# Performance work log

Hardware: AMD Instinct MI355X
Metric: run time of the kernel (lower is better)

Reference implementation:

```python
import jax, jax.numpy as jnp
import numpy as np

K = 3          # kernel_size
N = K * K      # sampling points per pixel
STRIDE = 1
PAD = 1
DIL = 1


def _conv2d(x, w, b):
    # standard NCHW conv for offset / modulation branches
    y = jax.lax.conv_general_dilated(
        x, w, window_strides=(STRIDE, STRIDE),
        padding=((PAD, PAD), (PAD, PAD)),
        rhs_dilation=(DIL, DIL),
        dimension_numbers=('NCHW', 'OIHW', 'NCHW'))
    return y + b[None, :, None, None]


def setup_inputs() -> dict:
    key = jax.random.key(0)
    ks = jax.random.split(key, 6)
    B, C, H, W, O = 8, 64, 96, 96, 64
    x = jax.random.normal(ks[0], (B, C, H, W), jnp.float32)
    # small random offset/modulation weights so sampling points are off-grid
    offset_w = jax.random.normal(ks[1], (2 * N, C, K, K), jnp.float32) * 0.01
    offset_b = jax.random.normal(ks[2], (2 * N,), jnp.float32) * 0.1
    m_w = jax.random.normal(ks[3], (N, C, K, K), jnp.float32) * 0.01
    m_b = jnp.zeros((N,), jnp.float32)
    # Conv3d(in=C, out=O, kernel=(1,1,N)) weight squeezed to [O, C, N]
    conv_w = jax.random.normal(ks[4], (O, C, N), jnp.float32) * (2.0 / (C * N)) ** 0.5
    conv_b = jnp.zeros((O,), jnp.float32)
    return dict(x=x, offset_w=offset_w, offset_b=offset_b,
                m_w=m_w, m_b=m_b, conv_w=conv_w, conv_b=conv_b)


def _deform_forward(x, offset_w, offset_b, m_w, m_b, conv_w, conv_b):
    B, C, H, W = x.shape
    offset = _conv2d(x, offset_w, offset_b)           # [B, 2n, h, w]
    m = jax.nn.sigmoid(_conv2d(x, m_w, m_b))          # [B, n, h, w]
    xp = jnp.pad(x, ((0, 0), (0, 0), (PAD, PAD), (PAD, PAD)))
    Hp, Wp = xp.shape[2], xp.shape[3]
    off = jnp.transpose(offset, (0, 2, 3, 1))         # [B, h, w, 2n]
    mod = jnp.transpose(m, (0, 2, 3, 1))              # [B, h, w, n]

    # p0: conv-center grid on the padded input; pn: kernel-tap offsets
    st = ((K - 1) // 2) * DIL
    p0_x = jnp.arange(st, Hp - (K // 2) * DIL, STRIDE, dtype=jnp.float32)  # [h]
    p0_y = jnp.arange(st, Wp - (K // 2) * DIL, STRIDE, dtype=jnp.float32)  # [w]
    r = jnp.arange(-((K - 1) // 2) * DIL, (K // 2) * DIL + 1, DIL, dtype=jnp.float32)
    pn_x, pn_y = jnp.meshgrid(r, r, indexing='ij')
    pn_x, pn_y = pn_x.reshape(N), pn_y.reshape(N)

    p_x = off[..., :N] + p0_x[None, :, None, None] + pn_x  # [B, h, w, n]
    p_y = off[..., N:] + p0_y[None, None, :, None] + pn_y

    fl_x = jnp.floor(jax.lax.stop_gradient(p_x))
    fl_y = jnp.floor(jax.lax.stop_gradient(p_y))
    q_tl_x = jnp.clip(fl_x, 0, Hp - 1).astype(jnp.int32)
    q_tl_y = jnp.clip(fl_y, 0, Wp - 1).astype(jnp.int32)
    q_br_x = jnp.clip(fl_x + 1, 0, Hp - 1).astype(jnp.int32)
    q_br_y = jnp.clip(fl_y + 1, 0, Wp - 1).astype(jnp.int32)

    pcx = jnp.clip(p_x, 0, Hp - 1)
    pcy = jnp.clip(p_y, 0, Wp - 1)

    tlx = q_tl_x.astype(pcx.dtype); tly = q_tl_y.astype(pcy.dtype)
    brx = q_br_x.astype(pcx.dtype); bry = q_br_y.astype(pcy.dtype)
    g_tl = (1 + (tlx - pcx)) * (1 + (tly - pcy))
    g_tr = (1 + (tlx - pcx)) * (1 - (bry - pcy))
    g_bl = (1 - (brx - pcx)) * (1 + (tly - pcy))
    g_br = (1 - (brx - pcx)) * (1 - (bry - pcy))

    xflat = xp.reshape(B, C, Hp * Wp)

    def gather(qx, qy):
        # per-batch gather: xf [C, Hp*Wp], idx [h, w, n] -> [C, h, w, n]
        return jax.vmap(lambda xf, i: xf[:, i])(xflat, qx * Wp + qy)

    xq_tl = gather(q_tl_x, q_tl_y)
    xq_tr = gather(q_tl_x, q_br_y)
    xq_bl = gather(q_br_x, q_tl_y)
    xq_br = gather(q_br_x, q_br_y)

    x_p = (g_tl[:, None] * xq_tl + g_tr[:, None] * xq_tr +
           g_bl[:, None] * xq_bl + g_br[:, None] * xq_br)
    x_p = x_p * mod[:, None]                           # modulation

    # Conv3d with (1,1,N) kernel == contraction over (C, N)
    out = jnp.einsum('bchwn,ocn->bohw', x_p, conv_w) + conv_b[None, :, None, None]
    return out


def reference(x, offset_w, offset_b, m_w, m_b, conv_w, conv_b):
    return _deform_forward(x, offset_w, offset_b, m_w, m_b, conv_w, conv_b)
```

## Files before the change

### kernel.cpp

```cpp
#include <hip/hip_runtime.h>
#include <hip/hip_fp16.h>
#include <cstddef>

#define B_   8
#define H_   96
#define W_   96
#define HW_  9216
#define PIX_ 73728

#define NWR    7
#define NWC    38
#define WINPX  266
#define NSLOTS 22

typedef __attribute__((ext_vector_type(8))) _Float16 halfx8;
typedef __attribute__((ext_vector_type(2))) __fp16 fp16x2_raw;
typedef __attribute__((ext_vector_type(4))) float floatx4;

#define XT_OFF   0
#define WFM_OFF  (XT_OFF + PIX_*64*2)
#define WFO_OFF  (WFM_OFF + 18*4*64*8*2)
#define WZ_OFF   (WFO_OFF + 18*2*64*8*2)

__device__ __forceinline__ unsigned pk2h(float a, float b) {
    fp16x2_raw h = __builtin_amdgcn_cvt_pkrtz(a, b);
    union { fp16x2_raw h2; unsigned u; } t; t.h2 = h; return t.u;
}
__device__ __forceinline__ halfx8 uph8(uint4 u) {
    union { uint4 u4; halfx8 h; } t; t.u4 = u; return t.h;
}
__device__ __forceinline__ halfx8 splat8(unsigned d) {
    union { unsigned u[4]; halfx8 h; } t;
    t.u[0] = d; t.u[1] = d; t.u[2] = d; t.u[3] = d; return t.h;
}
__device__ __forceinline__ void async_ld16(const void* g, void* l) {
    __builtin_amdgcn_global_load_lds((const __attribute__((address_space(1))) void*)g,
                                     (__attribute__((address_space(3))) void*)l,
                                     16, 0, 0);
}

__global__ __launch_bounds__(256) void k_transpose(const float* __restrict__ x,
                                                   unsigned short* __restrict__ xt,
                                                   const float* __restrict__ offw,
                                                   const float* __restrict__ mw,
                                                   const float* __restrict__ convw,
                                                   unsigned short* __restrict__ wfm,
                                                   unsigned short* __restrict__ wfo,
                                                   unsigned short* __restrict__ wz) {
    if (blockIdx.x >= 1152) {
        int g = (blockIdx.x - 1152) * 256 + threadIdx.x;
        if (g < 4608) {
            int lane = g & 63, mtks = g >> 6;
            int mt = mtks & 3, ks = mtks >> 2;
            int o = mt * 16 + (lane & 15), quad = lane >> 4;
            float v[8];
            #pragma unroll
            for (int j = 0; j < 8; ++j) {
                int k = ks * 32 + quad * 8 + j;
                int t = k / 64, c = k % 64;
                v[j] = convw[(size_t)(o * 64 + c) * 9 + t];
            }
            uint4 pk;
            pk.x = pk2h(v[0], v[1]); pk.y = pk2h(v[2], v[3]);
            pk.z = pk2h(v[4], v[5]); pk.w = pk2h(v[6], v[7]);
            *(uint4*)(wfm + (size_t)g * 8) = pk;
        } else if (g < 4608 + 2304) {
            int g2 = g - 4608;
            int lane = g2 & 63, mtks = g2 >> 6;
            int mt = mtks & 1, ks = mtks >> 1;
            int m = mt * 16 + (lane & 15), quad = lane >> 4;
            float v[8];
            #pragma unroll
            for (int j = 0; j < 8; ++j) {
                int k = ks * 32 + quad * 8 + j;
                int t = k / 64, c = k % 64;
                float f = 0.f;
                if (m < 18)      f = offw[(size_t)(m * 64 + c) * 9 + t];
                else if (m < 27) f = mw[(size_t)((m - 18) * 64 + c) * 9 + t];
                v[j] = f;
            }
            uint4 pk;
            pk.x = pk2h(v[0], v[1]); pk.y = pk2h(v[2], v[3]);
            pk.z = pk2h(v[4], v[5]); pk.w = pk2h(v[6], v[7]);
            *(uint4*)(wfo + (size_t)g2 * 8) = pk;
        } else if (g < 4608 + 2304 + 8) {
            uint4 z = make_uint4(0, 0, 0, 0);
            *(uint4*)(wz + (size_t)(g - 6912) * 8) = z;
        }
        return;
    }

    __shared__ float tile[64 * 65];
    int bb  = blockIdx.x / 144;
    int sp0 = (blockIdx.x % 144) * 64;
    int t = threadIdx.x;
    int s4 = (t & 15) * 4, cq = t >> 4;
    #pragma unroll
    for (int i = 0; i < 4; ++i) {
        int c = cq + 16 * i;
        float4 v = *(const float4*)&x[(size_t)(bb * 64 + c) * HW_ + sp0 + s4];
        tile[c * 65 + s4 + 0] = v.x;
        tile[c * 65 + s4 + 1] = v.y;
        tile[c * 65 + s4 + 2] = v.z;
        tile[c * 65 + s4 + 3] = v.w;
    }
    __syncthreads();
    int c8 = t & 7, sgrp = t >> 3;
    #pragma unroll
    for (int i = 0; i < 2; ++i) {
        int s2 = i * 32 + sgrp;
        uint4 pk;
        pk.x = pk2h(tile[(c8 * 8 + 0) * 65 + s2], tile[(c8 * 8 + 1) * 65 + s2]);
        pk.y = pk2h(tile[(c8 * 8 + 2) * 65 + s2], tile[(c8 * 8 + 3) * 65 + s2]);
        pk.z = pk2h(tile[(c8 * 8 + 4) * 65 + s2], tile[(c8 * 8 + 5) * 65 + s2]);
        pk.w = pk2h(tile[(c8 * 8 + 6) * 65 + s2], tile[(c8 * 8 + 7) * 65 + s2]);
        *(uint4*)(xt + (size_t)(bb * HW_ + sp0 + s2) * 64 + c8 * 8) = pk;
    }
}

__global__ __launch_bounds__(256, 3) void k_fused(const unsigned short* __restrict__ xt,
                                                  const unsigned short* __restrict__ wfo,
                                                  const unsigned short* __restrict__ wfm,
                                                  const float* __restrict__ offb,
                                                  const float* __restrict__ mb,
                                                  const float* __restrict__ convb,
                                                  const unsigned short* __restrict__ wz,
                                                  float* __restrict__ out) {
    __shared__ __align__(16) unsigned char s_win[(WINPX + NSLOTS) * 128];
    __shared__ float s_off[27 * 66];
    __shared__ __align__(16) unsigned char s_meta[64 * 9 * 16];
    __shared__ int s_cnt;

    int tid = threadIdx.x;
    int w = tid >> 6, lane = tid & 63, col = lane & 15, quad = lane >> 4;
    int blk = blockIdx.x;
    int bb  = blk / 144;
    int rem = blk % 144;
    int hr  = (rem / 3) * 2;
    int wc  = (rem % 3) * 32;
    const unsigned short* xtb = xt + (size_t)bb * HW_ * 64;

    if (tid == 0) s_cnt = 0;
    {
        int p0  = lane >> 3;
        int cgx = (lane & 7) ^ p0;
        const unsigned short* wzp = wz + cgx * 8;
        for (int i = w; i < 34; i += 4) {
            int p = i * 8 + p0;
            int wr = p / NWC, wcl = p - wr * NWC;
            int gr = hr - 2 + wr, gc = wc - 3 + wcl;
            bool ok = (p < WINPX) && ((unsigned)gr < 96u) && ((unsigned)gc < 96u);
            const unsigned short* src = ok ? (xtb + ((size_t)(gr * 96 + gc) * 64 + cgx * 8)) : wzp;
            async_ld16(src, s_win + i * 1024);
        }
    }
    __syncthreads();

    floatx4 aoff0 = (floatx4){0.f, 0.f, 0.f, 0.f};
    floatx4 aoff1 = (floatx4){0.f, 0.f, 0.f, 0.f};
    {
        int wr_base = 2 + (w >> 1);
        int wc_base = 3 + (w & 1) * 16 + col;
        #pragma unroll
        for (int t = 0; t < 9; ++t) {
            int dh = t / 3 - 1, dw = t % 3 - 1;
            int p = (wr_base + dh) * NWC + (wc_base + dw);
            int pb = p << 7, psw = (p & 7) << 4;
            #pragma unroll
            for (int ksl = 0; ksl < 2; ++ksl) {
                int ks = t * 2 + ksl;
                halfx8 a0 = *(const halfx8*)(wfo + ((size_t)(ks * 2 + 0) * 64 + lane) * 8);
                halfx8 a1 = *(const halfx8*)(wfo + ((size_t)(ks * 2 + 1) * 64 + lane) * 8);
                uint4 bvu = *(const uint4*)(s_win + pb + ((quad * 16 + ksl * 64) ^ psw));
                halfx8 bv = uph8(bvu);
                aoff0 = __builtin_amdgcn_mfma_f32_16x16x32_f16(a0, bv, aoff0, 0, 0, 0);
                aoff1 = __builtin_amdgcn_mfma_f32_16x16x32_f16(a1, bv, aoff1, 0, 0, 0);
            }
        }
    }
    #pragma unroll
    for (int r = 0; r < 4; ++r) {
        s_off[(quad * 4 + r) * 66 + (w * 16 + col)] = aoff0[r];
        int m = 16 + quad * 4 + r;
        if (m < 27) s_off[m * 66 + (w * 16 + col)] = aoff1[r];
    }
    __syncthreads();

    for (int id = tid; id < 576; id += 256) {
        int px = id & 63, n = id >> 6;
        float ox = s_off[n * 66 + px]        + offb[n];
        float oy = s_off[(9 + n) * 66 + px]  + offb[9 + n];
        float mv = s_off[(18 + n) * 66 + px] + mb[n];
        float modv = 1.f / (1.f + __expf(-mv));
        int prow = hr + (px >> 5), pcol = wc + (px & 31);
        float pxx = ox + (float)(prow + 1) + (float)(n / 3 - 1);
        float pyy = oy + (float)(pcol + 1) + (float)(n % 3 - 1);
        float flx = floorf(pxx), fly = floorf(pyy);
        float tlxf = fminf(fmaxf(flx,       0.f), 97.f);
        float tlyf = fminf(fmaxf(fly,       0.f), 97.f);
        float brxf = fminf(fmaxf(flx + 1.f, 0.f), 97.f);
        float bryf = fminf(fmaxf(fly + 1.f, 0.f), 97.f);
        float pcx  = fminf(fmaxf(pxx, 0.f), 97.f);
        float pcy  = fminf(fmaxf(pyy, 0.f), 97.f);
        float gx0 = 1.f + tlxf - pcx;
        float gx1 = 1.f - (brxf - pcx);
        float gy0 = 1.f + tlyf - pcy;
        float gy1 = 1.f - (bryf - pcy);
        int tlx = (int)tlxf, tly = (int)tlyf, brx = (int)brxf, bry = (int)bryf;
        int   qxs[4] = {tlx, tlx, brx, brx};
        int   qys[4] = {tly, bry, tly, bry};
        float gs4[4] = {gx0 * gy0, gx0 * gy1, gx1 * gy0, gx1 * gy1};
        unsigned short si[4]; unsigned short hg[4];
        #pragma unroll
        for (int c4 = 0; c4 < 4; ++c4) {
            int qx = qxs[c4], qy = qys[c4];
            bool valid = (qx >= 1) && (qx <= 96) && (qy >= 1) && (qy <= 96);
            int gr = qx - 1, gc = qy - 1;
            int wr = gr - (hr - 2), wcl = gc - (wc - 3);
            bool inwin = ((unsigned)wr < (unsigned)NWR) && ((unsigned)wcl < (unsigned)NWC);
            unsigned short idxv; float gvf;
            if (inwin) {
                idxv = (unsigned short)(wr * NWC + wcl);
                gvf = gs4[c4] * modv;
            } else if (!valid) {
                idxv = 0; gvf = 0.f;
            } else {
                int s = atomicAdd(&s_cnt, 1);
                int gidx = gr * 96 + gc;
                if (s < NSLOTS) {
                    int ps = WINPX + s;
                    #pragma unroll
                    for (int ch = 0; ch < 8; ++ch) {
                        uint4 v = *(const uint4*)(xtb + (size_t)gidx * 64 + ch * 8);
                        *(uint4*)(s_win + (size_t)ps * 128 + ((ch ^ (ps & 7)) * 16)) = v;
                    }
                    idxv = (unsigned short)ps;
                } else {
                    idxv = (unsigned short)(0x8000u | (unsigned)gidx);
                }
                gvf = gs4[c4] * modv;
            }
            si[c4] = idxv;
            hg[c4] = __half_as_ushort(__float2half_rn(gvf));
        }
        uint4 mw4;
        mw4.x = si[0] | ((unsigned)si[1] << 16);
        mw4.y = si[2] | ((unsigned)si[3] << 16);
        mw4.z = hg[0] | ((unsigned)hg[1] << 16);
        mw4.w = hg[2] | ((unsigned)hg[3] << 16);
        *(uint4*)(s_meta + ((size_t)px * 9 + n) * 16) = mw4;
    }
    __syncthreads();

    int mth = w & 1, pg = w >> 1;
    floatx4 acc[2][2];
    #pragma unroll
    for (int jj = 0; jj < 2; ++jj)
        #pragma unroll
        for (int mtl = 0; mtl < 2; ++mtl) acc[jj][mtl] = (floatx4){0.f, 0.f, 0.f, 0.f};

    int qk0 = quad * 16, qk1 = quad * 16 + 64;

    #pragma unroll
    for (int n = 0; n < 9; ++n) {
        halfx8 af00 = *(const halfx8*)(wfm + ((size_t)((n * 2 + 0) * 4 + mth * 2 + 0) * 64 + lane) * 8);
        halfx8 af01 = *(const halfx8*)(wfm + ((size_t)((n * 2 + 0) * 4 + mth * 2 + 1) * 64 + lane) * 8);
        halfx8 af10 = *(const halfx8*)(wfm + ((size_t)((n * 2 + 1) * 4 + mth * 2 + 0) * 64 + lane) * 8);
        halfx8 af11 = *(const halfx8*)(wfm + ((size_t)((n * 2 + 1) * 4 + mth * 2 + 1) * 64 + lane) * 8);
        #pragma unroll
        for (int jj = 0; jj < 2; ++jj) {
            int px = pg * 32 + jj * 16 + col;
            uint4 mu = *(const uint4*)(s_meta + ((size_t)px * 9 + n) * 16);
            unsigned i0 = mu.x & 0xFFFFu, i1 = mu.x >> 16;
            unsigned i2 = mu.y & 0xFFFFu, i3 = mu.y >> 16;
            int pm0 = (i0 & 0x8000u) ? 0 : (int)i0;
            int pm1 = (i1 & 0x8000u) ? 0 : (int)i1;
            int pm2 = (i2 & 0x8000u) ? 0 : (int)i2;
            int pm3 = (i3 & 0x8000u) ? 0 : (int)i3;
            int b0 = pm0 << 7, s0 = (pm0 & 7) << 4;
            int b1 = pm1 << 7, s1 = (pm1 & 7) << 4;
            int b2 = pm2 << 7, s2 = (pm2 & 7) << 4;
            int b3 = pm3 << 7, s3 = (pm3 & 7) << 4;
            uint4 cA0 = *(const uint4*)(s_win + b0 + (qk0 ^ s0));
            uint4 cA1 = *(const uint4*)(s_win + b1 + (qk0 ^ s1));
            uint4 cA2 = *(const uint4*)(s_win + b2 + (qk0 ^ s2));
            uint4 cA3 = *(const uint4*)(s_win + b3 + (qk0 ^ s3));
            uint4 cB0 = *(const uint4*)(s_win + b0 + (qk1 ^ s0));
            uint4 cB1 = *(const uint4*)(s_win + b1 + (qk1 ^ s1));
            uint4 cB2 = *(const uint4*)(s_win + b2 + (qk1 ^ s2));
            uint4 cB3 = *(const uint4*)(s_win + b3 + (qk1 ^ s3));
            if (__any((int)((i0 | i1 | i2 | i3) & 0x8000u))) {
                if (i0 & 0x8000u) { size_t ga = (size_t)(i0 & 0x3FFFu) * 64 + quad * 8;
                    cA0 = *(const uint4*)(xtb + ga); cB0 = *(const uint4*)(xtb + ga + 32); }
                if (i1 & 0x8000u) { size_t ga = (size_t)(i1 & 0x3FFFu) * 64 + quad * 8;
                    cA1 = *(const uint4*)(xtb + ga); cB1 = *(const uint4*)(xtb + ga + 32); }
                if (i2 & 0x8000u) { size_t ga = (size_t)(i2 & 0x3FFFu) * 64 + quad * 8;
                    cA2 = *(const uint4*)(xtb + ga); cB2 = *(const uint4*)(xtb + ga + 32); }
                if (i3 & 0x8000u) { size_t ga = (size_t)(i3 & 0x3FFFu) * 64 + quad * 8;
                    cA3 = *(const uint4*)(xtb + ga); cB3 = *(const uint4*)(xtb + ga + 32); }
            }
            unsigned gl0 = (mu.z & 0xFFFFu) | (mu.z << 16);
            unsigned gl1 = (mu.z >> 16) | (mu.z & 0xFFFF0000u);
            unsigned gl2 = (mu.w & 0xFFFFu) | (mu.w << 16);
            unsigned gl3 = (mu.w >> 16) | (mu.w & 0xFFFF0000u);
            halfx8 g0 = splat8(gl0), g1 = splat8(gl1), g2 = splat8(gl2), g3 = splat8(gl3);
            halfx8 vA = uph8(cA0) * g0;
            vA += uph8(cA1) * g1; vA += uph8(cA2) * g2; vA += uph8(cA3) * g3;
            halfx8 vB = uph8(cB0) * g0;
            vB += uph8(cB1) * g1; vB += uph8(cB2) * g2; vB += uph8(cB3) * g3;
            acc[jj][0] = __builtin_amdgcn_mfma_f32_16x16x32_f16(af00, vA, acc[jj][0], 0, 0, 0);
            acc[jj][1] = __builtin_amdgcn_mfma_f32_16x16x32_f16(af01, vA, acc[jj][1], 0, 0, 0);
            acc[jj][0] = __builtin_amdgcn_mfma_f32_16x16x32_f16(af10, vB, acc[jj][0], 0, 0, 0);
            acc[jj][1] = __builtin_amdgcn_mfma_f32_16x16x32_f16(af11, vB, acc[jj][1], 0, 0, 0);
        }
    }

    int prow = hr + pg;
    #pragma unroll
    for (int mtl = 0; mtl < 2; ++mtl) {
        float4 cb4 = *(const float4*)&convb[mth * 32 + mtl * 16 + quad * 4];
        #pragma unroll
        for (int jj = 0; jj < 2; ++jj) {
            int sp = prow * 96 + wc + jj * 16 + col;
            #pragma unroll
            for (int r = 0; r < 4; ++r) {
                int o = mth * 32 + mtl * 16 + quad * 4 + r;
                float bias = (r == 0) ? cb4.x : (r == 1) ? cb4.y : (r == 2) ? cb4.z : cb4.w;
                out[(size_t)(bb * 64 + o) * HW_ + sp] = acc[jj][mtl][r] + bias;
            }
        }
    }
}

extern "C" void kernel_launch(void* const* d_in, const int* in_sizes, int n_in,
                              void* d_out, int out_size, void* d_ws, size_t ws_size,
                              hipStream_t stream) {
    const float* x     = (const float*)d_in[0];
    const float* offw  = (const float*)d_in[1];
    const float* offb  = (const float*)d_in[2];
    const float* mw    = (const float*)d_in[3];
    const float* mb    = (const float*)d_in[4];
    const float* convw = (const float*)d_in[5];
    const float* convb = (const float*)d_in[6];
    char* ws = (char*)d_ws;
    unsigned short* xt16 = (unsigned short*)(ws + XT_OFF);
    unsigned short* wfm  = (unsigned short*)(ws + WFM_OFF);
    unsigned short* wfo  = (unsigned short*)(ws + WFO_OFF);
    unsigned short* wz   = (unsigned short*)(ws + WZ_OFF);
    float* out = (float*)d_out;

    k_transpose<<<dim3(1152 + 28), dim3(256), 0, stream>>>(x, xt16, offw, mw, convw, wfm, wfo, wz);
    k_fused    <<<dim3(1152),      dim3(256), 0, stream>>>(xt16, wfo, wfm, offb, mb, convb, wz, out);
}
```

Measured before the change: 115.7 us.

## Shrink LDS footprint to fit four blocks per CU and swizzle block order

Cuts the staged input window from 7 to 6 rows with fewer overflow slots. It also aliases the offset buffer and the sampling-metadata buffer in one shared region, adding an extra barrier after the offsets are read into registers. This lowers LDS use so launch bounds can ask for 4 blocks per CU instead of 3. The block index is also remapped so that consecutive blocks come from different batches. The smaller window may push more off-window samples to the global-memory fallback path, and the tighter occupancy target may cost registers.

```diff
diff --git a/kernel.cpp b/kernel.cpp
--- a/kernel.cpp
+++ b/kernel.cpp
@@ -8,10 +8,10 @@
 #define HW_  9216
 #define PIX_ 73728
 
-#define NWR    7
+#define NWR    6
 #define NWC    38
-#define WINPX  266
-#define NSLOTS 22
+#define WINPX  228
+#define NSLOTS 19
 
 typedef __attribute__((ext_vector_type(8))) _Float16 halfx8;
 typedef __attribute__((ext_vector_type(2))) __fp16 fp16x2_raw;
@@ -118,7 +118,7 @@
     }
 }
 
-__global__ __launch_bounds__(256, 3) void k_fused(const unsigned short* __restrict__ xt,
+__global__ __launch_bounds__(256, 4) void k_fused(const unsigned short* __restrict__ xt,
                                                   const unsigned short* __restrict__ wfo,
                                                   const unsigned short* __restrict__ wfm,
                                                   const float* __restrict__ offb,
@@ -127,13 +127,14 @@
                                                   const unsigned short* __restrict__ wz,
                                                   float* __restrict__ out) {
     __shared__ __align__(16) unsigned char s_win[(WINPX + NSLOTS) * 128];
-    __shared__ float s_off[27 * 66];
-    __shared__ __align__(16) unsigned char s_meta[64 * 9 * 16];
+    __shared__ __align__(16) unsigned char s_u[9216];
     __shared__ int s_cnt;
+    float* s_off = (float*)s_u;
+    unsigned char* s_meta = s_u;
 
     int tid = threadIdx.x;
     int w = tid >> 6, lane = tid & 63, col = lane & 15, quad = lane >> 4;
-    int blk = blockIdx.x;
+    int blk = (blockIdx.x & 7) * 144 + (blockIdx.x >> 3);
     int bb  = blk / 144;
     int rem = blk % 144;
     int hr  = (rem / 3) * 2;
@@ -145,7 +146,7 @@
         int p0  = lane >> 3;
         int cgx = (lane & 7) ^ p0;
         const unsigned short* wzp = wz + cgx * 8;
-        for (int i = w; i < 34; i += 4) {
+        for (int i = w; i < 29; i += 4) {
             int p = i * 8 + p0;
             int wr = p / NWC, wcl = p - wr * NWC;
             int gr = hr - 2 + wr, gc = wc - 3 + wcl;
@@ -186,11 +187,32 @@
     }
     __syncthreads();
 
-    for (int id = tid; id < 576; id += 256) {
+    float ox0, oy0, mv0, ox1, oy1, mv1, ox2 = 0.f, oy2 = 0.f, mv2 = 0.f;
+    bool has2 = (tid + 512) < 576;
+    {
+        int px = tid & 63, n = tid >> 6;
+        ox0 = s_off[n * 66 + px]        + offb[n];
+        oy0 = s_off[(9 + n) * 66 + px]  + offb[9 + n];
+        mv0 = s_off[(18 + n) * 66 + px] + mb[n];
+    }
+    {
+        int id = tid + 256;
         int px = id & 63, n = id >> 6;
-        float ox = s_off[n * 66 + px]        + offb[n];
-        float oy = s_off[(9 + n) * 66 + px]  + offb[9 + n];
-        float mv = s_off[(18 + n) * 66 + px] + mb[n];
+        ox1 = s_off[n * 66 + px]        + offb[n];
+        oy1 = s_off[(9 + n) * 66 + px]  + offb[9 + n];
+        mv1 = s_off[(18 + n) * 66 + px] + mb[n];
+    }
+    if (has2) {
+        int id = tid + 512;
+        int px = id & 63, n = id >> 6;
+        ox2 = s_off[n * 66 + px]        + offb[n];
+        oy2 = s_off[(9 + n) * 66 + px]  + offb[9 + n];
+        mv2 = s_off[(18 + n) * 66 + px] + mb[n];
+    }
+    __syncthreads();
+
+    auto meta_one = [&](int id, float ox, float oy, float mv) {
+        int px = id & 63, n = id >> 6;
         float modv = 1.f / (1.f + __expf(-mv));
         int prow = hr + (px >> 5), pcol = wc + (px & 31);
         float pxx = ox + (float)(prow + 1) + (float)(n / 3 - 1);
@@ -249,7 +271,10 @@
         mw4.z = hg[0] | ((unsigned)hg[1] << 16);
         mw4.w = hg[2] | ((unsigned)hg[3] << 16);
         *(uint4*)(s_meta + ((size_t)px * 9 + n) * 16) = mw4;
-    }
+    };
+    meta_one(tid,       ox0, oy0, mv0);
+    meta_one(tid + 256, ox1, oy1, mv1);
+    if (has2) meta_one(tid + 512, ox2, oy2, mv2);
     __syncthreads();
 
     int mth = w & 1, pg = w >> 1;
```

Measured after the change: 113.3 us. -2.1%, faster.
